# Optimization experiments

Hardware: AMD Instinct MI355X
Metric: run time of the kernel (lower is better)

## Reference

```python
import jax, jax.numpy as jnp
import numpy as np

BATCH, SEQ, IN_DIM, UNITS = 64, 2048, 256, 256


def _glorot(key, shape):
    lim = np.sqrt(6.0 / (shape[0] + shape[1]))
    return jax.random.uniform(key, shape, jnp.float32, -lim, lim)


def setup_inputs() -> dict:
    key = jax.random.key(0)
    ks = jax.random.split(key, 5)
    return {
        "inputs": jax.random.normal(ks[0], (BATCH, SEQ, IN_DIM), jnp.float32),
        "W_f": _glorot(ks[1], (IN_DIM, UNITS)),
        "U_f": _glorot(ks[2], (UNITS, UNITS)),
        "b_f": jnp.zeros((UNITS,), jnp.float32),
        "W_s": _glorot(ks[3], (IN_DIM, UNITS)),
        "U_s": _glorot(ks[4], (UNITS, UNITS)),
        "b_s": jnp.zeros((UNITS,), jnp.float32),
    }


def reference(inputs, W_f, U_f, b_f, W_s, U_s, b_s):
    # Precompute input projections for all timesteps (one big GEMM each).
    xf = jnp.einsum('bti,iu->btu', inputs, W_f) + b_f  # (B, T, U)
    xs = jnp.einsum('bti,iu->btu', inputs, W_s) + b_s  # (B, T, U)

    h0 = jnp.zeros((inputs.shape[0], U_f.shape[0]), inputs.dtype)

    def step(h, xt):
        xf_t, xs_t = xt
        f_t = jax.nn.sigmoid(xf_t + h @ U_f)
        s_tilde = jnp.tanh(xs_t + (f_t * h) @ U_s)
        h_new = (1.0 - f_t) * h + f_t * s_tilde
        return h_new, h_new

    # scan over time: move time axis to front
    _, hs = jax.lax.scan(step, h0, (jnp.swapaxes(xf, 0, 1), jnp.swapaxes(xs, 0, 1)))
    return jnp.swapaxes(hs, 0, 1)  # (B, T, U)
```

## Files before the change

### kernel.cpp

```cpp
#include <hip/hip_runtime.h>
#include <hip/hip_bf16.h>

#define BATCH 64
#define SEQ 2048
#define IN_DIM 256
#define UNITS 256

typedef _Float16 half2_t __attribute__((ext_vector_type(2)));

__device__ __forceinline__ float fdot2(half2_t a, half2_t b, float c) {
#if __has_builtin(__builtin_amdgcn_fdot2)
    return __builtin_amdgcn_fdot2(a, b, c, false);
#else
    return c + (float)a[0] * (float)b[0] + (float)a[1] * (float)b[1];
#endif
}

__global__ void prep_u(const float* __restrict__ Uf, const float* __restrict__ Us,
                       _Float16* __restrict__ Utf, _Float16* __restrict__ Uts) {
    int idx = blockIdx.x * 256 + threadIdx.x;
    int k = idx >> 8;
    int u = idx & 255;
    Utf[u * 256 + k] = (_Float16)Uf[idx];
    Uts[u * 256 + k] = (_Float16)Us[idx];
}

__global__ __launch_bounds__(256) void proj_kernel(
    const float* __restrict__ X,
    const float* __restrict__ Wf, const float* __restrict__ bf,
    const float* __restrict__ Wsm, const float* __restrict__ bs,
    float* __restrict__ xf_out, _Float16* __restrict__ xs_out)
{
    __shared__ float Xs[64][65];
    __shared__ float Wsh[64][68];

    const int tid = threadIdx.x;
    const int rt = blockIdx.x;
    const int ct = blockIdx.y;
    const int r0 = rt * 64;
    const bool is_f = ct < 4;
    const int c0 = (ct & 3) * 64;
    const float* W = is_f ? Wf : Wsm;
    const float* bias = is_f ? bf : bs;
    const int tx = tid & 15;
    const int ty = tid >> 4;

    float acc[4][4];
#pragma unroll
    for (int i = 0; i < 4; ++i)
#pragma unroll
        for (int j = 0; j < 4; ++j) acc[i][j] = 0.f;

    for (int kc = 0; kc < IN_DIM; kc += 64) {
        __syncthreads();
#pragma unroll
        for (int i = 0; i < 4; ++i) {
            int f = tid + i * 256;
            int row = f >> 4;
            int kq = f & 15;
            float4 v = *(const float4*)(X + (size_t)(r0 + row) * IN_DIM + kc + kq * 4);
            Xs[row][kq * 4 + 0] = v.x;
            Xs[row][kq * 4 + 1] = v.y;
            Xs[row][kq * 4 + 2] = v.z;
            Xs[row][kq * 4 + 3] = v.w;
        }
#pragma unroll
        for (int i = 0; i < 4; ++i) {
            int f = tid + i * 256;
            int kk = f >> 4;
            int n4 = f & 15;
            float4 v = *(const float4*)(W + (size_t)(kc + kk) * UNITS + c0 + n4 * 4);
            *(float4*)&Wsh[kk][n4 * 4] = v;
        }
        __syncthreads();
#pragma unroll 8
        for (int kk = 0; kk < 64; ++kk) {
            float a0 = Xs[tx * 4 + 0][kk];
            float a1 = Xs[tx * 4 + 1][kk];
            float a2 = Xs[tx * 4 + 2][kk];
            float a3 = Xs[tx * 4 + 3][kk];
            float4 bv = *(const float4*)&Wsh[kk][ty * 4];
            acc[0][0] += a0 * bv.x; acc[0][1] += a0 * bv.y; acc[0][2] += a0 * bv.z; acc[0][3] += a0 * bv.w;
            acc[1][0] += a1 * bv.x; acc[1][1] += a1 * bv.y; acc[1][2] += a1 * bv.z; acc[1][3] += a1 * bv.w;
            acc[2][0] += a2 * bv.x; acc[2][1] += a2 * bv.y; acc[2][2] += a2 * bv.z; acc[2][3] += a2 * bv.w;
            acc[3][0] += a3 * bv.x; acc[3][1] += a3 * bv.y; acc[3][2] += a3 * bv.z; acc[3][3] += a3 * bv.w;
        }
    }

#pragma unroll
    for (int i = 0; i < 4; ++i) {
        int r = r0 + tx * 4 + i;
        int n0 = c0 + ty * 4;
        if (is_f) {
            float4 v;
            v.x = acc[i][0] + bias[n0 + 0];
            v.y = acc[i][1] + bias[n0 + 1];
            v.z = acc[i][2] + bias[n0 + 2];
            v.w = acc[i][3] + bias[n0 + 3];
            *(float4*)(xf_out + (size_t)r * UNITS + n0) = v;
        } else {
#pragma unroll
            for (int j = 0; j < 4; ++j)
                xs_out[(size_t)r * UNITS + n0 + j] = (_Float16)(acc[i][j] + bias[n0 + j]);
        }
    }
}

__global__ __launch_bounds__(1024) void recur_kernel(
    float* xf_out,
    const _Float16* __restrict__ xs16,
    const _Float16* __restrict__ Utf,
    const _Float16* __restrict__ Uts)
{
    __shared__ float part[4][256];
    __shared__ float hbuf[256];
    __shared__ float fbuf[256];
    __shared__ __align__(16) _Float16 h2[256];
    __shared__ __align__(16) _Float16 g2[256];

    const int tid = threadIdx.x;
    const int u = tid & 255;
    const int q = tid >> 8;
    const int b = blockIdx.x;

    union F4H { float4 f4; half2_t h[4]; };

    half2_t uf[32], us[32];
    {
        const float4* pf = (const float4*)(Utf + ((size_t)u * 256 + q * 64));
        const float4* ps = (const float4*)(Uts + ((size_t)u * 256 + q * 64));
#pragma unroll
        for (int j = 0; j < 8; ++j) {
            F4H a; a.f4 = pf[j];
            F4H c; c.f4 = ps[j];
#pragma unroll
            for (int m = 0; m < 4; ++m) {
                uf[4 * j + m] = a.h[m];
                us[4 * j + m] = c.h[m];
            }
        }
    }

    if (tid < 256) {
        hbuf[tid] = 0.f;
        h2[tid] = (_Float16)0.f;
    }
    __syncthreads();

    const size_t base = (size_t)b * SEQ * UNITS;

    for (int t = 0; t < SEQ; ++t) {
        float xfv = 0.f, xsv = 0.f;
        if (tid < 256) {
            xfv = xf_out[base + (size_t)t * UNITS + tid];
            xsv = (float)xs16[base + (size_t)t * UNITS + tid];
        }

        {
            const float4* hv4 = (const float4*)h2;
            float a0 = 0.f, a1 = 0.f, a2 = 0.f, a3 = 0.f;
#pragma unroll
            for (int j = 0; j < 8; ++j) {
                F4H hh; hh.f4 = hv4[8 * q + j];
                a0 = fdot2(uf[4 * j + 0], hh.h[0], a0);
                a1 = fdot2(uf[4 * j + 1], hh.h[1], a1);
                a2 = fdot2(uf[4 * j + 2], hh.h[2], a2);
                a3 = fdot2(uf[4 * j + 3], hh.h[3], a3);
            }
            part[q][u] = (a0 + a1) + (a2 + a3);
        }
        __syncthreads();

        if (tid < 256) {
            float sum = (part[0][tid] + part[1][tid]) + (part[2][tid] + part[3][tid]);
            float f = 1.f / (1.f + __expf(-(xfv + sum)));
            fbuf[tid] = f;
            g2[tid] = (_Float16)(f * hbuf[tid]);
        }
        __syncthreads();

        {
            const float4* gv4 = (const float4*)g2;
            float a0 = 0.f, a1 = 0.f, a2 = 0.f, a3 = 0.f;
#pragma unroll
            for (int j = 0; j < 8; ++j) {
                F4H hh; hh.f4 = gv4[8 * q + j];
                a0 = fdot2(us[4 * j + 0], hh.h[0], a0);
                a1 = fdot2(us[4 * j + 1], hh.h[1], a1);
                a2 = fdot2(us[4 * j + 2], hh.h[2], a2);
                a3 = fdot2(us[4 * j + 3], hh.h[3], a3);
            }
            part[q][u] = (a0 + a1) + (a2 + a3);
        }
        __syncthreads();

        if (tid < 256) {
            float sum = (part[0][tid] + part[1][tid]) + (part[2][tid] + part[3][tid]);
            float z = xsv + sum;
            z = fminf(fmaxf(z, -15.f), 15.f);
            float e = __expf(2.f * z);
            float s = (e - 1.f) / (e + 1.f);
            float f = fbuf[tid];
            float hv = hbuf[tid];
            float hn = (1.f - f) * hv + f * s;
            hbuf[tid] = hn;
            h2[tid] = (_Float16)hn;
            xf_out[base + (size_t)t * UNITS + tid] = hn;
        }
        __syncthreads();
    }
}

extern "C" void kernel_launch(void* const* d_in, const int* in_sizes, int n_in,
                              void* d_out, int out_size, void* d_ws, size_t ws_size,
                              hipStream_t stream) {
    (void)in_sizes; (void)n_in; (void)out_size; (void)ws_size;

    const float* X   = (const float*)d_in[0];
    const float* Wf  = (const float*)d_in[1];
    const float* Uf  = (const float*)d_in[2];
    const float* bf  = (const float*)d_in[3];
    const float* Wsm = (const float*)d_in[4];
    const float* Us  = (const float*)d_in[5];
    const float* bs  = (const float*)d_in[6];
    float* out = (float*)d_out;

    _Float16* xs16 = (_Float16*)d_ws;
    _Float16* Utf  = xs16 + (size_t)BATCH * SEQ * UNITS;
    _Float16* Uts  = Utf + 256 * 256;

    prep_u<<<256, 256, 0, stream>>>(Uf, Us, Utf, Uts);
    proj_kernel<<<dim3(BATCH * SEQ / 64, 8), 256, 0, stream>>>(X, Wf, bf, Wsm, bs, out, xs16);
    recur_kernel<<<BATCH, 1024, 0, stream>>>(out, xs16, Utf, Uts);
}
```

Measured before the change: 3.508 ms.

## Restructure recurrent matvec with DPP row reductions and register-held state

The recurrent kernel now assigns each 16-lane row four output units and reduces the k-dimension partial sums with DPP cross-lane adds. This replaces the shared-memory partial buffer and its 4-way reduction. The h/g vectors are stored in padded shared layout to avoid bank conflicts. Hidden state and gate are kept in registers, and the next timestep's xf/xs inputs are prefetched to hide global load latency on the serial critical path. The extra DPP steps and the reliance on row_shr/bcast semantics add reduction latency and correctness risk.

```diff
diff --git a/kernel.cpp b/kernel.cpp
--- a/kernel.cpp
+++ b/kernel.cpp
@@ -14,6 +14,19 @@
 #else
     return c + (float)a[0] * (float)b[0] + (float)a[1] * (float)b[1];
 #endif
+}
+
+template <int CTRL>
+__device__ __forceinline__ float dpp_xor_add(float v) {
+    int s = __builtin_amdgcn_update_dpp(0, __float_as_int(v), CTRL, 0xF, 0xF, true);
+    return v + __int_as_float(s);
+}
+__device__ __forceinline__ float row16_sum(float v) {
+    v = dpp_xor_add<0xB1>(v);
+    v = dpp_xor_add<0x4E>(v);
+    v = dpp_xor_add<0x141>(v);
+    v = dpp_xor_add<0x140>(v);
+    return v;
 }
 
 __global__ void prep_u(const float* __restrict__ Uf, const float* __restrict__ Us,
@@ -112,100 +125,130 @@
     const _Float16* __restrict__ Utf,
     const _Float16* __restrict__ Uts)
 {
-    __shared__ float part[4][256];
-    __shared__ float hbuf[256];
-    __shared__ float fbuf[256];
-    __shared__ __align__(16) _Float16 h2[256];
-    __shared__ __align__(16) _Float16 g2[256];
+    __shared__ __align__(16) _Float16 h2p[16 * 24];
+    __shared__ __align__(16) _Float16 g2p[16 * 24];
+    __shared__ float sumf[256];
+    __shared__ float sums[256];
 
     const int tid = threadIdx.x;
-    const int u = tid & 255;
-    const int q = tid >> 8;
+    const int w = tid >> 6;
+    const int lane = tid & 63;
+    const int g = lane & 15;
+    const int r = lane >> 4;
+    const int u0 = 16 * w + 4 * r;
     const int b = blockIdx.x;
 
     union F4H { float4 f4; half2_t h[4]; };
 
-    half2_t uf[32], us[32];
-    {
-        const float4* pf = (const float4*)(Utf + ((size_t)u * 256 + q * 64));
-        const float4* ps = (const float4*)(Uts + ((size_t)u * 256 + q * 64));
-#pragma unroll
-        for (int j = 0; j < 8; ++j) {
-            F4H a; a.f4 = pf[j];
-            F4H c; c.f4 = ps[j];
-#pragma unroll
-            for (int m = 0; m < 4; ++m) {
-                uf[4 * j + m] = a.h[m];
-                us[4 * j + m] = c.h[m];
-            }
-        }
-    }
-
+    half2_t uf[4][8], us[4][8];
+#pragma unroll
+    for (int i = 0; i < 4; ++i) {
+        const float4* pf = (const float4*)(Utf + ((size_t)(u0 + i) * 256 + 16 * g));
+        const float4* ps = (const float4*)(Uts + ((size_t)(u0 + i) * 256 + 16 * g));
+        F4H a0; a0.f4 = pf[0];
+        F4H a1; a1.f4 = pf[1];
+        F4H c0; c0.f4 = ps[0];
+        F4H c1; c1.f4 = ps[1];
+#pragma unroll
+        for (int m = 0; m < 4; ++m) {
+            uf[i][m] = a0.h[m];
+            uf[i][4 + m] = a1.h[m];
+            us[i][m] = c0.h[m];
+            us[i][4 + m] = c1.h[m];
+        }
+    }
+
+    if (tid < 16 * 24) h2p[tid] = (_Float16)0.f;
+
+    const size_t base = (size_t)b * SEQ * UNITS;
+
+    float h_old = 0.f, f_gate = 0.f;
+    float xf_cur = 0.f, xs_cur = 0.f;
     if (tid < 256) {
-        hbuf[tid] = 0.f;
-        h2[tid] = (_Float16)0.f;
+        xf_cur = xf_out[base + tid];
+        xs_cur = (float)xs16[base + tid];
     }
     __syncthreads();
 
-    const size_t base = (size_t)b * SEQ * UNITS;
-
     for (int t = 0; t < SEQ; ++t) {
-        float xfv = 0.f, xsv = 0.f;
+        const int tn = (t + 1 < SEQ) ? t + 1 : t;
+
+        {
+            const float4* hv4 = (const float4*)(h2p + g * 24);
+            F4H h0; h0.f4 = hv4[0];
+            F4H h1; h1.f4 = hv4[1];
+            float a0 = 0.f, a1 = 0.f, a2 = 0.f, a3 = 0.f;
+#pragma unroll
+            for (int m = 0; m < 4; ++m) {
+                a0 = fdot2(uf[0][m], h0.h[m], a0);
+                a1 = fdot2(uf[1][m], h0.h[m], a1);
+                a2 = fdot2(uf[2][m], h0.h[m], a2);
+                a3 = fdot2(uf[3][m], h0.h[m], a3);
+            }
+#pragma unroll
+            for (int m = 0; m < 4; ++m) {
+                a0 = fdot2(uf[0][4 + m], h1.h[m], a0);
+                a1 = fdot2(uf[1][4 + m], h1.h[m], a1);
+                a2 = fdot2(uf[2][4 + m], h1.h[m], a2);
+                a3 = fdot2(uf[3][4 + m], h1.h[m], a3);
+            }
+            a0 = row16_sum(a0); a1 = row16_sum(a1);
+            a2 = row16_sum(a2); a3 = row16_sum(a3);
+            if (g == 0) {
+                float4 v; v.x = a0; v.y = a1; v.z = a2; v.w = a3;
+                *(float4*)(sumf + u0) = v;
+            }
+        }
+        __syncthreads();
+
+        float xf_nxt = 0.f;
         if (tid < 256) {
-            xfv = xf_out[base + (size_t)t * UNITS + tid];
-            xsv = (float)xs16[base + (size_t)t * UNITS + tid];
-        }
+            float f = 1.f / (1.f + __expf(-(xf_cur + sumf[tid])));
+            f_gate = f;
+            g2p[(tid >> 4) * 24 + (tid & 15)] = (_Float16)(f * h_old);
+            xf_nxt = xf_out[base + (size_t)tn * UNITS + tid];
+        }
+        __syncthreads();
 
         {
-            const float4* hv4 = (const float4*)h2;
+            const float4* gv4 = (const float4*)(g2p + g * 24);
+            F4H h0; h0.f4 = gv4[0];
+            F4H h1; h1.f4 = gv4[1];
             float a0 = 0.f, a1 = 0.f, a2 = 0.f, a3 = 0.f;
 #pragma unroll
-            for (int j = 0; j < 8; ++j) {
-                F4H hh; hh.f4 = hv4[8 * q + j];
-                a0 = fdot2(uf[4 * j + 0], hh.h[0], a0);
-                a1 = fdot2(uf[4 * j + 1], hh.h[1], a1);
-                a2 = fdot2(uf[4 * j + 2], hh.h[2], a2);
-                a3 = fdot2(uf[4 * j + 3], hh.h[3], a3);
-            }
-            part[q][u] = (a0 + a1) + (a2 + a3);
+            for (int m = 0; m < 4; ++m) {
+                a0 = fdot2(us[0][m], h0.h[m], a0);
+                a1 = fdot2(us[1][m], h0.h[m], a1);
+                a2 = fdot2(us[2][m], h0.h[m], a2);
+                a3 = fdot2(us[3][m], h0.h[m], a3);
+            }
+#pragma unroll
+            for (int m = 0; m < 4; ++m) {
+                a0 = fdot2(us[0][4 + m], h1.h[m], a0);
+                a1 = fdot2(us[1][4 + m], h1.h[m], a1);
+                a2 = fdot2(us[2][4 + m], h1.h[m], a2);
+                a3 = fdot2(us[3][4 + m], h1.h[m], a3);
+            }
+            a0 = row16_sum(a0); a1 = row16_sum(a1);
+            a2 = row16_sum(a2); a3 = row16_sum(a3);
+            if (g == 0) {
+                float4 v; v.x = a0; v.y = a1; v.z = a2; v.w = a3;
+                *(float4*)(sums + u0) = v;
+            }
         }
         __syncthreads();
 
         if (tid < 256) {
-            float sum = (part[0][tid] + part[1][tid]) + (part[2][tid] + part[3][tid]);
-            float f = 1.f / (1.f + __expf(-(xfv + sum)));
-            fbuf[tid] = f;
-            g2[tid] = (_Float16)(f * hbuf[tid]);
-        }
-        __syncthreads();
-
-        {
-            const float4* gv4 = (const float4*)g2;
-            float a0 = 0.f, a1 = 0.f, a2 = 0.f, a3 = 0.f;
-#pragma unroll
-            for (int j = 0; j < 8; ++j) {
-                F4H hh; hh.f4 = gv4[8 * q + j];
-                a0 = fdot2(us[4 * j + 0], hh.h[0], a0);
-                a1 = fdot2(us[4 * j + 1], hh.h[1], a1);
-                a2 = fdot2(us[4 * j + 2], hh.h[2], a2);
-                a3 = fdot2(us[4 * j + 3], hh.h[3], a3);
-            }
-            part[q][u] = (a0 + a1) + (a2 + a3);
-        }
-        __syncthreads();
-
-        if (tid < 256) {
-            float sum = (part[0][tid] + part[1][tid]) + (part[2][tid] + part[3][tid]);
-            float z = xsv + sum;
+            float z = xs_cur + sums[tid];
             z = fminf(fmaxf(z, -15.f), 15.f);
             float e = __expf(2.f * z);
             float s = (e - 1.f) / (e + 1.f);
-            float f = fbuf[tid];
-            float hv = hbuf[tid];
-            float hn = (1.f - f) * hv + f * s;
-            hbuf[tid] = hn;
-            h2[tid] = (_Float16)hn;
+            float hn = (1.f - f_gate) * h_old + f_gate * s;
+            h_old = hn;
+            h2p[(tid >> 4) * 24 + (tid & 15)] = (_Float16)hn;
             xf_out[base + (size_t)t * UNITS + tid] = hn;
+            xf_cur = xf_nxt;
+            xs_cur = (float)xs16[base + (size_t)tn * UNITS + tid];
         }
         __syncthreads();
     }
```

New measurement: 4.085 ms. 1.16x slower.

## Restructure recurrent step with DPP row reductions and two barriers per timestep

Applied to the files above, without the earlier changes.

Each recurrent timestep now assigns two output units to each row of 8 lanes and reduces the K-split partial dot products with DPP cross-lane adds instead of a shared-memory partial array. The number of barriers per step drops from four to two, using a lightweight s_waitcnt+s_barrier macro. Hidden state, gate values and the next timestep's projected inputs are kept in registers, and the next inputs are prefetched one step ahead. The h/g vectors are stored in padded shared memory to avoid bank conflicts. The aim is to shorten the serial per-step latency, at the cost of relying on DPP row semantics and inline asm barriers.

```diff
diff --git a/kernel.cpp b/kernel.cpp
--- a/kernel.cpp
+++ b/kernel.cpp
@@ -15,6 +15,20 @@
     return c + (float)a[0] * (float)b[0] + (float)a[1] * (float)b[1];
 #endif
 }
+
+template <int CTRL>
+__device__ __forceinline__ float dpp_xor_add(float v) {
+    int s = __builtin_amdgcn_update_dpp(0, __float_as_int(v), CTRL, 0xF, 0xF, true);
+    return v + __int_as_float(s);
+}
+__device__ __forceinline__ float row8_sum(float v) {
+    v = dpp_xor_add<0xB1>(v);
+    v = dpp_xor_add<0x4E>(v);
+    v = dpp_xor_add<0x141>(v);
+    return v;
+}
+
+#define BAR() asm volatile("s_waitcnt lgkmcnt(0)\n\ts_barrier" ::: "memory")
 
 __global__ void prep_u(const float* __restrict__ Uf, const float* __restrict__ Us,
                        _Float16* __restrict__ Utf, _Float16* __restrict__ Uts) {
@@ -112,102 +126,133 @@
     const _Float16* __restrict__ Utf,
     const _Float16* __restrict__ Uts)
 {
-    __shared__ float part[4][256];
-    __shared__ float hbuf[256];
-    __shared__ float fbuf[256];
-    __shared__ __align__(16) _Float16 h2[256];
-    __shared__ __align__(16) _Float16 g2[256];
+    __shared__ __align__(16) _Float16 h2p[8 * 40];
+    __shared__ __align__(16) _Float16 g2p[8 * 40];
 
     const int tid = threadIdx.x;
-    const int u = tid & 255;
-    const int q = tid >> 8;
+    const int w = tid >> 6;
+    const int lane = tid & 63;
+    const int g = lane & 7;
+    const int r = lane >> 3;
+    const int u0 = 16 * w + 2 * r;
     const int b = blockIdx.x;
 
     union F4H { float4 f4; half2_t h[4]; };
-
-    half2_t uf[32], us[32];
-    {
-        const float4* pf = (const float4*)(Utf + ((size_t)u * 256 + q * 64));
-        const float4* ps = (const float4*)(Uts + ((size_t)u * 256 + q * 64));
-#pragma unroll
-        for (int j = 0; j < 8; ++j) {
-            F4H a; a.f4 = pf[j];
-            F4H c; c.f4 = ps[j];
+    union U2H { unsigned u; half2_t h; };
+
+    half2_t uf[2][16], us[2][16];
+#pragma unroll
+    for (int i = 0; i < 2; ++i) {
+        const float4* pf = (const float4*)(Utf + ((size_t)(u0 + i) * 256 + 32 * g));
+        const float4* ps = (const float4*)(Uts + ((size_t)(u0 + i) * 256 + 32 * g));
+#pragma unroll
+        for (int jj = 0; jj < 4; ++jj) {
+            F4H a; a.f4 = pf[jj];
+            F4H c; c.f4 = ps[jj];
 #pragma unroll
             for (int m = 0; m < 4; ++m) {
-                uf[4 * j + m] = a.h[m];
-                us[4 * j + m] = c.h[m];
-            }
-        }
-    }
-
-    if (tid < 256) {
-        hbuf[tid] = 0.f;
-        h2[tid] = (_Float16)0.f;
+                uf[i][4 * jj + m] = a.h[m];
+                us[i][4 * jj + m] = c.h[m];
+            }
+        }
+    }
+
+    if (tid < 8 * 40) h2p[tid] = (_Float16)0.f;
+
+    const size_t base = (size_t)b * SEQ * UNITS;
+    const int widx = (w >> 1) * 40 + 16 * (w & 1) + 2 * r;
+
+    float h_old0 = 0.f, h_old1 = 0.f, f0 = 0.f, f1 = 0.f;
+    float2 xf_cur = make_float2(0.f, 0.f);
+    unsigned xs_cur = 0;
+    if (g == 0) {
+        xf_cur = *(const float2*)(xf_out + base + u0);
+        xs_cur = *(const unsigned*)(xs16 + base + u0);
     }
     __syncthreads();
 
-    const size_t base = (size_t)b * SEQ * UNITS;
-
     for (int t = 0; t < SEQ; ++t) {
-        float xfv = 0.f, xsv = 0.f;
-        if (tid < 256) {
-            xfv = xf_out[base + (size_t)t * UNITS + tid];
-            xsv = (float)xs16[base + (size_t)t * UNITS + tid];
+        const int tn = (t + 1 < SEQ) ? t + 1 : t;
+
+        float2 xf_nxt = make_float2(0.f, 0.f);
+        unsigned xs_nxt = 0;
+        if (g == 0) {
+            xf_nxt = *(const float2*)(xf_out + base + (size_t)tn * UNITS + u0);
+            xs_nxt = *(const unsigned*)(xs16 + base + (size_t)tn * UNITS + u0);
         }
 
         {
-            const float4* hv4 = (const float4*)h2;
-            float a0 = 0.f, a1 = 0.f, a2 = 0.f, a3 = 0.f;
-#pragma unroll
-            for (int j = 0; j < 8; ++j) {
-                F4H hh; hh.f4 = hv4[8 * q + j];
-                a0 = fdot2(uf[4 * j + 0], hh.h[0], a0);
-                a1 = fdot2(uf[4 * j + 1], hh.h[1], a1);
-                a2 = fdot2(uf[4 * j + 2], hh.h[2], a2);
-                a3 = fdot2(uf[4 * j + 3], hh.h[3], a3);
-            }
-            part[q][u] = (a0 + a1) + (a2 + a3);
-        }
-        __syncthreads();
-
-        if (tid < 256) {
-            float sum = (part[0][tid] + part[1][tid]) + (part[2][tid] + part[3][tid]);
-            float f = 1.f / (1.f + __expf(-(xfv + sum)));
-            fbuf[tid] = f;
-            g2[tid] = (_Float16)(f * hbuf[tid]);
-        }
-        __syncthreads();
+            const float4* hv = (const float4*)(h2p + g * 40);
+            F4H H0, H1, H2, H3;
+            H0.f4 = hv[0]; H1.f4 = hv[1]; H2.f4 = hv[2]; H3.f4 = hv[3];
+            float a0 = 0.f, a1 = 0.f;
+#pragma unroll
+            for (int m = 0; m < 4; ++m) {
+                a0 = fdot2(uf[0][m +  0], H0.h[m], a0);
+                a1 = fdot2(uf[1][m +  0], H0.h[m], a1);
+                a0 = fdot2(uf[0][m +  4], H1.h[m], a0);
+                a1 = fdot2(uf[1][m +  4], H1.h[m], a1);
+                a0 = fdot2(uf[0][m +  8], H2.h[m], a0);
+                a1 = fdot2(uf[1][m +  8], H2.h[m], a1);
+                a0 = fdot2(uf[0][m + 12], H3.h[m], a0);
+                a1 = fdot2(uf[1][m + 12], H3.h[m], a1);
+            }
+            a0 = row8_sum(a0);
+            a1 = row8_sum(a1);
+            if (g == 0) {
+                f0 = 1.f / (1.f + __expf(-(xf_cur.x + a0)));
+                f1 = 1.f / (1.f + __expf(-(xf_cur.y + a1)));
+                half2_t gv;
+                gv[0] = (_Float16)(f0 * h_old0);
+                gv[1] = (_Float16)(f1 * h_old1);
+                *(half2_t*)(g2p + widx) = gv;
+            }
+        }
+        BAR();
 
         {
-            const float4* gv4 = (const float4*)g2;
-            float a0 = 0.f, a1 = 0.f, a2 = 0.f, a3 = 0.f;
-#pragma unroll
-            for (int j = 0; j < 8; ++j) {
-                F4H hh; hh.f4 = gv4[8 * q + j];
-                a0 = fdot2(us[4 * j + 0], hh.h[0], a0);
-                a1 = fdot2(us[4 * j + 1], hh.h[1], a1);
-                a2 = fdot2(us[4 * j + 2], hh.h[2], a2);
-                a3 = fdot2(us[4 * j + 3], hh.h[3], a3);
-            }
-            part[q][u] = (a0 + a1) + (a2 + a3);
-        }
-        __syncthreads();
-
-        if (tid < 256) {
-            float sum = (part[0][tid] + part[1][tid]) + (part[2][tid] + part[3][tid]);
-            float z = xsv + sum;
-            z = fminf(fmaxf(z, -15.f), 15.f);
-            float e = __expf(2.f * z);
-            float s = (e - 1.f) / (e + 1.f);
-            float f = fbuf[tid];
-            float hv = hbuf[tid];
-            float hn = (1.f - f) * hv + f * s;
-            hbuf[tid] = hn;
-            h2[tid] = (_Float16)hn;
-            xf_out[base + (size_t)t * UNITS + tid] = hn;
-        }
-        __syncthreads();
+            const float4* gv4 = (const float4*)(g2p + g * 40);
+            F4H G0, G1, G2, G3;
+            G0.f4 = gv4[0]; G1.f4 = gv4[1]; G2.f4 = gv4[2]; G3.f4 = gv4[3];
+            float c0 = 0.f, c1 = 0.f;
+#pragma unroll
+            for (int m = 0; m < 4; ++m) {
+                c0 = fdot2(us[0][m +  0], G0.h[m], c0);
+                c1 = fdot2(us[1][m +  0], G0.h[m], c1);
+                c0 = fdot2(us[0][m +  4], G1.h[m], c0);
+                c1 = fdot2(us[1][m +  4], G1.h[m], c1);
+                c0 = fdot2(us[0][m +  8], G2.h[m], c0);
+                c1 = fdot2(us[1][m +  8], G2.h[m], c1);
+                c0 = fdot2(us[0][m + 12], G3.h[m], c0);
+                c1 = fdot2(us[1][m + 12], G3.h[m], c1);
+            }
+            c0 = row8_sum(c0);
+            c1 = row8_sum(c1);
+            if (g == 0) {
+                U2H xh; xh.u = xs_cur;
+                float z0 = (float)xh.h[0] + c0;
+                float z1 = (float)xh.h[1] + c1;
+                z0 = fminf(fmaxf(z0, -15.f), 15.f);
+                z1 = fminf(fmaxf(z1, -15.f), 15.f);
+                float e0 = __expf(2.f * z0);
+                float e1 = __expf(2.f * z1);
+                float s0 = 1.f - 2.f / (e0 + 1.f);
+                float s1 = 1.f - 2.f / (e1 + 1.f);
+                float hn0 = h_old0 + f0 * (s0 - h_old0);
+                float hn1 = h_old1 + f1 * (s1 - h_old1);
+                h_old0 = hn0;
+                h_old1 = hn1;
+                half2_t hv2;
+                hv2[0] = (_Float16)hn0;
+                hv2[1] = (_Float16)hn1;
+                *(half2_t*)(h2p + widx) = hv2;
+                float2 st; st.x = hn0; st.y = hn1;
+                *(float2*)(xf_out + base + (size_t)t * UNITS + u0) = st;
+                xf_cur = xf_nxt;
+                xs_cur = xs_nxt;
+            }
+        }
+        BAR();
     }
 }
 
```

Result: slower. 4.266 ms (+21.6%).
